# Performance work log

Measured on AMD Instinct MI355X. Metric: run time of the kernel, lower is better.

## Reference

```python
import jax, jax.numpy as jnp
import numpy as np

B, L, D_MODEL, H, HD, FD = 1, 1024, 1024, 16, 64, 64
EPS = 1e-12

def setup_inputs() -> dict:
    key = jax.random.key(0)
    ks = jax.random.split(key, 7)
    s = 1.0 / np.sqrt(D_MODEL)
    return {
        'x': jax.random.normal(ks[0], (B, L, D_MODEL), jnp.float32),
        'Wq': jax.random.normal(ks[1], (D_MODEL, H * HD), jnp.float32) * s,
        'Wk': jax.random.normal(ks[2], (D_MODEL, H * HD), jnp.float32) * s,
        'Wv': jax.random.normal(ks[3], (D_MODEL, H * HD), jnp.float32) * s,
        'Wo': jax.random.normal(ks[4], (H * HD, D_MODEL), jnp.float32) * s,
        'Kq': jax.random.normal(ks[5], (H, HD, FD), jnp.float32) * (1.0 / np.sqrt(HD)),
        'Kk': jax.random.normal(ks[6], (H, HD, FD), jnp.float32) * (1.0 / np.sqrt(HD)),
    }

def _heads(t):
    # (b, l, h*d) -> (b, h, l, d)
    b, l, _ = t.shape
    return t.reshape(b, l, H, HD).transpose(0, 2, 1, 3)

def _feature_map(t, K):
    # UntiedHeadEinsumMLP (no skip) + SoftmaxDim with temp=1.0
    f = jnp.einsum('hdf,bhld->bhlf', K, t)
    feats = jnp.concatenate([jax.nn.softmax(f, axis=-1), jax.nn.softmax(-f, axis=-1)], axis=-1)
    return jnp.maximum(feats, EPS)  # clamp(min=eps)

def reference(x, Wq, Wk, Wv, Wo, Kq, Kk):
    q = _heads(x @ Wq)  # b h l d
    k = _heads(x @ Wk)
    v = _heads(x @ Wv)
    qf = _feature_map(q, Kq)  # b h l 2f
    kf = _feature_map(k, Kk)  # b h l 2f
    # causal linear attention: o_t = phi(q_t) . sum_{s<=t} phi(k_s) v_s^T, normalized
    kv = jnp.cumsum(kf[:, :, :, None, :] * v[..., None], axis=2)  # b h l d 2f
    o = jnp.einsum('bhlf,bhldf->bhld', qf, kv)
    z = jnp.einsum('bhlf,bhlf->bhl', qf, jnp.cumsum(kf, axis=2)) + EPS
    o = o / z[..., None]
    y = o.transpose(0, 2, 1, 3).reshape(x.shape[0], x.shape[1], H * HD)
    return y @ Wo
```

## Files before the change

### kernel.cpp

```cpp
#include <hip/hip_runtime.h>
#include <hip/hip_bf16.h>


#define NH 16
#define NC 16

using short8 = __attribute__((ext_vector_type(8))) short;
using f32x4  = __attribute__((ext_vector_type(4))) float;
typedef const __attribute__((address_space(1))) char* gptr1;
typedef __attribute__((address_space(3))) char* lptr3;

static __device__ __forceinline__ unsigned short bf16bits(float x) {
    __hip_bfloat16 h = __float2bfloat16(x);
    return __builtin_bit_cast(unsigned short, h);
}
static __device__ __forceinline__ float b2f(unsigned short u) {
    return __builtin_bit_cast(float, (unsigned int)u << 16);
}
#define SWZ(row, cb) ((cb) ^ (((row) & 7) << 4))

template<int RS>
static __device__ __forceinline__ short8 ldfrag(const char* buf, int row, int kelem) {
    return *(const short8*)(buf + row * RS + SWZ(row, kelem * 2));
}

__global__ __launch_bounds__(256) void prep(const float* __restrict__ x,
                                            const float* __restrict__ w0,
                                            const float* __restrict__ w1,
                                            const float* __restrict__ w2,
                                            const float* __restrict__ w3,
                                            const float* __restrict__ Kq,
                                            const float* __restrict__ Kk,
                                            __hip_bfloat16* __restrict__ xb,
                                            __hip_bfloat16* __restrict__ d0,
                                            __hip_bfloat16* __restrict__ d1,
                                            __hip_bfloat16* __restrict__ d2,
                                            __hip_bfloat16* __restrict__ d3,
                                            __hip_bfloat16* __restrict__ KqT,
                                            __hip_bfloat16* __restrict__ KkT) {
    const int z = blockIdx.z;
    const int tx = threadIdx.x, ty = threadIdx.y;
    const int tid = ty * 32 + tx;
    if (z < 4) {
        const float* src = (z == 0) ? w0 : (z == 1) ? w1 : (z == 2) ? w2 : w3;
        __hip_bfloat16* dst = (z == 0) ? d0 : (z == 1) ? d1 : (z == 2) ? d2 : d3;
        __shared__ float tile[32][33];
        const int bx = blockIdx.x * 32, by = blockIdx.y * 32;
#pragma unroll
        for (int i = 0; i < 32; i += 8)
            tile[ty + i][tx] = src[(by + ty + i) * 1024 + bx + tx];
        __syncthreads();
#pragma unroll
        for (int i = 0; i < 32; i += 8)
            dst[(size_t)(bx + ty + i) * 1024 + by + tx] = __float2bfloat16(tile[tx][ty + i]);
    } else if (z == 4) {
        const int blk = blockIdx.y * 32 + blockIdx.x;
        const int i = (blk * 256 + tid) * 4;
        float4 v = *(const float4*)(x + i);
        ushort4 o;
        o.x = bf16bits(v.x); o.y = bf16bits(v.y); o.z = bf16bits(v.z); o.w = bf16bits(v.w);
        *(ushort4*)((unsigned short*)xb + i) = o;
    } else {
        if (blockIdx.y != 0 || blockIdx.x >= 32) return;
        const int h = blockIdx.x & 15;
        const float* S = (blockIdx.x >> 4) ? Kk : Kq;
        __hip_bfloat16* D = (blockIdx.x >> 4) ? KkT : KqT;
        __shared__ float t[64][65];
#pragma unroll
        for (int j = 0; j < 16; j++) {
            int e = tid + j * 256, r = e >> 6, c = e & 63;
            t[r][c] = S[h * 4096 + r * 64 + c];
        }
        __syncthreads();
#pragma unroll
        for (int j = 0; j < 16; j++) {
            int e = tid + j * 256, r = e >> 6, c = e & 63;
            D[h * 4096 + r * 64 + c] = __float2bfloat16(t[c][r]);
        }
    }
}

__global__ __launch_bounds__(256) void qkv_feat(const __hip_bfloat16* __restrict__ A,
                                                const __hip_bfloat16* __restrict__ B0,
                                                const __hip_bfloat16* __restrict__ B1,
                                                const __hip_bfloat16* __restrict__ B2,
                                                const __hip_bfloat16* __restrict__ KqT,
                                                const __hip_bfloat16* __restrict__ KkT,
                                                __hip_bfloat16* __restrict__ qf,
                                                __hip_bfloat16* __restrict__ kf,
                                                __hip_bfloat16* __restrict__ kfT,
                                                __hip_bfloat16* __restrict__ VT) {
    __shared__ __align__(16) char smem[49152];
    const int tid = threadIdx.x;
    const int bm = blockIdx.y * 128;
    const int which = blockIdx.x >> 4;
    const int h = blockIdx.x & 15;
    const __hip_bfloat16* B = (which == 0) ? B0 : (which == 1) ? B1 : B2;
    const int bn = h * 64;
    const int wid = tid >> 6, lane = tid & 63;
    const int g = lane >> 4, r16 = lane & 15;
    const char* Ab = (const char*)A;
    const char* Bb = (const char*)B;
    f32x4 acc[2][4] = {};

#define QKV_STAGE(dstA, dstB, kbyte)                                                                   \
    do {                                                                                               \
        _Pragma("unroll") for (int it = 0; it < 4; it++) {                                             \
            const int off = it * 4096 + tid * 16;                                                      \
            const int row = off >> 7, cb = off & 127;                                                  \
            __builtin_amdgcn_global_load_lds((gptr1)(Ab + (size_t)(bm + row) * 2048 + (kbyte) + SWZ(row, cb)), \
                                             (lptr3)((dstA) + it * 4096 + wid * 1024), 16, 0, 0);      \
        }                                                                                              \
        _Pragma("unroll") for (int it = 0; it < 2; it++) {                                             \
            const int off = it * 4096 + tid * 16;                                                      \
            const int row = off >> 7, cb = off & 127;                                                  \
            __builtin_amdgcn_global_load_lds((gptr1)(Bb + (size_t)(bn + row) * 2048 + (kbyte) + SWZ(row, cb)), \
                                             (lptr3)((dstB) + it * 4096 + wid * 1024), 16, 0, 0);      \
        }                                                                                              \
    } while (0)

    QKV_STAGE(smem, smem + 32768, 0);
    for (int kt = 0; kt < 16; kt++) {
        char* Ac = smem + ((kt & 1) ? 16384 : 0);
        char* Bc = smem + 32768 + ((kt & 1) ? 8192 : 0);
        if (kt < 15) {
            char* An = smem + ((kt & 1) ? 0 : 16384);
            char* Bn = smem + 32768 + ((kt & 1) ? 0 : 8192);
            QKV_STAGE(An, Bn, (kt + 1) * 128);
            asm volatile("s_waitcnt vmcnt(6)" ::: "memory");
        } else {
            asm volatile("s_waitcnt vmcnt(0)" ::: "memory");
        }
        __builtin_amdgcn_s_barrier();
#pragma unroll
        for (int ks = 0; ks < 2; ks++) {
            short8 af[2], bfr[4];
#pragma unroll
            for (int m = 0; m < 2; m++)
                af[m] = ldfrag<128>(Ac, wid * 32 + m * 16 + r16, ks * 32 + g * 8);
#pragma unroll
            for (int n = 0; n < 4; n++)
                bfr[n] = ldfrag<128>(Bc, n * 16 + r16, ks * 32 + g * 8);
#pragma unroll
            for (int m = 0; m < 2; m++)
#pragma unroll
                for (int n = 0; n < 4; n++)
                    acc[m][n] = __builtin_amdgcn_mfma_f32_16x16x32_bf16(af[m], bfr[n], acc[m][n], 0, 0, 0);
        }
        asm volatile("s_waitcnt lgkmcnt(0)" ::: "memory");
        __builtin_amdgcn_s_barrier();
    }
#undef QKV_STAGE

    if (which == 2) {
#pragma unroll
        for (int m = 0; m < 2; m++)
#pragma unroll
            for (int n = 0; n < 4; n++) {
                const int col = bn + n * 16 + r16;
                const int row0 = bm + wid * 32 + m * 16 + g * 4;
                ushort4 v;
                v.x = bf16bits(acc[m][n][0]); v.y = bf16bits(acc[m][n][1]);
                v.z = bf16bits(acc[m][n][2]); v.w = bf16bits(acc[m][n][3]);
                *(ushort4*)((unsigned short*)VT + (size_t)col * 1024 + row0) = v;
            }
        return;
    }

    const bool kside = (which == 1);
    char* XS = smem + 32768;
#pragma unroll
    for (int m = 0; m < 2; m++)
#pragma unroll
        for (int n = 0; n < 4; n++)
#pragma unroll
            for (int i = 0; i < 4; i++) {
                const int row = wid * 32 + m * 16 + g * 4 + i;
                *(unsigned short*)(XS + row * 128 + SWZ(row, (n * 16 + r16) * 2)) = bf16bits(acc[m][n][i]);
            }
    {
        const char* KTp = (const char*)(kside ? KkT : KqT);
#pragma unroll
        for (int it = 0; it < 2; it++) {
            const int off = it * 4096 + tid * 16;
            const int row = off >> 7, cb = off & 127;
            __builtin_amdgcn_global_load_lds((gptr1)(KTp + (size_t)(h * 64 + row) * 128 + SWZ(row, cb)),
                                             (lptr3)(smem + it * 4096 + wid * 1024), 16, 0, 0);
        }
    }
    __syncthreads();

    f32x4 fr[2][4] = {};
#pragma unroll
    for (int ks = 0; ks < 2; ks++) {
        short8 af[2], bfr[4];
#pragma unroll
        for (int m = 0; m < 2; m++)
            af[m] = ldfrag<128>(XS, wid * 32 + m * 16 + r16, ks * 32 + g * 8);
#pragma unroll
        for (int n = 0; n < 4; n++)
            bfr[n] = ldfrag<128>(smem, n * 16 + r16, ks * 32 + g * 8);
#pragma unroll
        for (int m = 0; m < 2; m++)
#pragma unroll
            for (int n = 0; n < 4; n++)
                fr[m][n] = __builtin_amdgcn_mfma_f32_16x16x32_bf16(af[m], bfr[n], fr[m][n], 0, 0, 0);
    }
    if (kside) __syncthreads();

    char* ft = smem;
    __hip_bfloat16* feat = kside ? kf : qf;
#pragma unroll
    for (int m = 0; m < 2; m++)
#pragma unroll
        for (int i = 0; i < 4; i++) {
            const int row = wid * 32 + m * 16 + g * 4 + i;
            float m1 = fr[m][0][i], m2 = -fr[m][0][i];
#pragma unroll
            for (int n = 1; n < 4; n++) {
                m1 = fmaxf(m1, fr[m][n][i]);
                m2 = fmaxf(m2, -fr[m][n][i]);
            }
#pragma unroll
            for (int off = 8; off; off >>= 1) {
                m1 = fmaxf(m1, __shfl_xor(m1, off));
                m2 = fmaxf(m2, __shfl_xor(m2, off));
            }
            float e1[4], e2[4], s1 = 0.f, s2 = 0.f;
#pragma unroll
            for (int n = 0; n < 4; n++) {
                e1[n] = __expf(fr[m][n][i] - m1);  s1 += e1[n];
                e2[n] = __expf(-fr[m][n][i] - m2); s2 += e2[n];
            }
#pragma unroll
            for (int off = 8; off; off >>= 1) {
                s1 += __shfl_xor(s1, off);
                s2 += __shfl_xor(s2, off);
            }
            const float i1 = 1.f / s1, i2 = 1.f / s2;
            __hip_bfloat16* fo = feat + ((size_t)(h * 1024 + bm + row)) * 128;
#pragma unroll
            for (int n = 0; n < 4; n++) {
                const int col = n * 16 + r16;
                unsigned short v1 = bf16bits(fmaxf(e1[n] * i1, 1e-12f));
                unsigned short v2 = bf16bits(fmaxf(e2[n] * i2, 1e-12f));
                *(unsigned short*)(fo + col) = v1;
                *(unsigned short*)(fo + col + 64) = v2;
                if (kside) {
                    *(unsigned short*)(ft + col * 256 + SWZ(col, row * 2)) = v1;
                    *(unsigned short*)(ft + (col + 64) * 256 + SWZ(col + 64, row * 2)) = v2;
                }
            }
        }
    if (kside) {
        __syncthreads();
#pragma unroll
        for (int j = 0; j < 8; j++) {
            const int off = (tid + j * 256) * 16;
            const int row = off >> 8, cb = off & 255;
            short8 v = *(const short8*)(ft + row * 256 + SWZ(row, cb));
            *(short8*)((char*)kfT + ((size_t)(h * 128 + row) * 1024 + bm) * 2 + cb) = v;
        }
    }
}

__global__ __launch_bounds__(256) void chunk_sums_mfma(const __hip_bfloat16* __restrict__ kfT,
                                                       const __hip_bfloat16* __restrict__ VT,
                                                       __hip_bfloat16* __restrict__ Scb,
                                                       float* __restrict__ ksum) {
    const int h = blockIdx.y, c = blockIdx.x, l0 = c * 64;
    __shared__ __align__(16) char VTs[64 * 128];
    __shared__ __align__(16) char KTs[128 * 128];
    const int tid = threadIdx.x, lane = tid & 63, wid = tid >> 6;
    const int r16 = lane & 15, g = lane >> 4;
#pragma unroll
    for (int it = 0; it < 2; it++) {
        const int off = it * 4096 + tid * 16;
        const int row = off >> 7, cb = off & 127;
        __builtin_amdgcn_global_load_lds((gptr1)((const char*)VT + ((size_t)(h * 64 + row) * 1024 + l0) * 2 + SWZ(row, cb)),
                                         (lptr3)(VTs + it * 4096 + wid * 1024), 16, 0, 0);
    }
#pragma unroll
    for (int it = 0; it < 4; it++) {
        const int off = it * 4096 + tid * 16;
        const int row = off >> 7, cb = off & 127;
        __builtin_amdgcn_global_load_lds((gptr1)((const char*)kfT + ((size_t)(h * 128 + row) * 1024 + l0) * 2 + SWZ(row, cb)),
                                         (lptr3)(KTs + it * 4096 + wid * 1024), 16, 0, 0);
    }
    __syncthreads();
    f32x4 acc[8] = {};
#pragma unroll
    for (int ks = 0; ks < 2; ks++) {
        short8 a = ldfrag<128>(VTs, wid * 16 + r16, ks * 32 + g * 8);
#pragma unroll
        for (int n = 0; n < 8; n++) {
            short8 b = ldfrag<128>(KTs, n * 16 + r16, ks * 32 + g * 8);
            acc[n] = __builtin_amdgcn_mfma_f32_16x16x32_bf16(a, b, acc[n], 0, 0, 0);
        }
    }
    unsigned short* o = (unsigned short*)Scb + (size_t)(h * NC + c) * 8192;
#pragma unroll
    for (int n = 0; n < 8; n++)
#pragma unroll
        for (int i = 0; i < 4; i++)
            o[(wid * 16 + g * 4 + i) * 128 + n * 16 + r16] = bf16bits(acc[n][i]);
    if (tid < 128) {
        float s = 0.f;
#pragma unroll 8
        for (int t = 0; t < 64; t++)
            s += b2f(*(const unsigned short*)(KTs + tid * 128 + SWZ(tid, t * 2)));
        ksum[(size_t)(h * NC + c) * 128 + tid] = s;
    }
}

__global__ __launch_bounds__(256) void prefix_scan(const __hip_bfloat16* __restrict__ Scb,
                                                   __hip_bfloat16* __restrict__ Sp,
                                                   const float* __restrict__ ksum,
                                                   float* __restrict__ kp) {
    const int h = blockIdx.x, eb = blockIdx.y, tid = threadIdx.x;
#pragma unroll
    for (int j = 0; j < 4; j++) {
        const int e = eb * 1024 + tid + j * 256;
        float v[NC];
#pragma unroll
        for (int c = 0; c < NC; c++)
            v[c] = b2f(((const unsigned short*)Scb)[(size_t)(h * NC + c) * 8192 + e]);
        float run = 0.f;
#pragma unroll
        for (int c = 0; c < NC; c++) {
            Sp[(size_t)(h * NC + c) * 8192 + e] = __float2bfloat16(run);
            run += v[c];
        }
    }
    if (eb == 0 && tid < 128) {
        float run = 0.f;
#pragma unroll
        for (int c = 0; c < NC; c++) {
            const size_t idx = (size_t)(h * NC + c) * 128 + tid;
            kp[idx] = run;
            run += ksum[idx];
        }
    }
}

__global__ __launch_bounds__(256) void chunk_out_mfma(const __hip_bfloat16* __restrict__ qf,
                                                      const __hip_bfloat16* __restrict__ kf,
                                                      const __hip_bfloat16* __restrict__ VT,
                                                      const __hip_bfloat16* __restrict__ Sp,
                                                      const float* __restrict__ kp,
                                                      __hip_bfloat16* __restrict__ Y) {
    const int h = blockIdx.y, c = blockIdx.x, l0 = c * 64;
    __shared__ __align__(16) char QF[64 * 256];
    __shared__ __align__(16) char KF[64 * 256];
    __shared__ __align__(16) char SP[64 * 256];
    __shared__ __align__(16) char VTs[64 * 128];
    __shared__ __align__(16) char AM[64 * 128];
    __shared__ float zi[64];
    __shared__ float invz[64];
    const int tid = threadIdx.x, lane = tid & 63, wid = tid >> 6;
    const int r16 = lane & 15, g = lane >> 4;

#pragma unroll
    for (int it = 0; it < 4; it++) {
        const int off = it * 4096 + wid * 1024 + lane * 16;
        const int row = off >> 8, cb = off & 255;
        const int sw = SWZ(row, cb);
        __builtin_amdgcn_global_load_lds((gptr1)((const char*)qf + ((size_t)(h * 1024 + l0 + row)) * 256 + sw),
                                         (lptr3)(QF + it * 4096 + wid * 1024), 16, 0, 0);
        __builtin_amdgcn_global_load_lds((gptr1)((const char*)kf + ((size_t)(h * 1024 + l0 + row)) * 256 + sw),
                                         (lptr3)(KF + it * 4096 + wid * 1024), 16, 0, 0);
        __builtin_amdgcn_global_load_lds((gptr1)((const char*)Sp + ((size_t)((h * NC + c) * 64 + row)) * 256 + sw),
                                         (lptr3)(SP + it * 4096 + wid * 1024), 16, 0, 0);
    }
#pragma unroll
    for (int it = 0; it < 2; it++) {
        const int off = it * 4096 + wid * 1024 + lane * 16;
        const int row = off >> 7, cb = off & 127;
        __builtin_amdgcn_global_load_lds((gptr1)((const char*)VT + ((size_t)(h * 64 + row) * 1024 + l0) * 2 + SWZ(row, cb)),
                                         (lptr3)(VTs + it * 4096 + wid * 1024), 16, 0, 0);
    }
    __syncthreads();

    f32x4 a4[4] = {};
#pragma unroll
    for (int ks = 0; ks < 4; ks++) {
        short8 a = ldfrag<256>(QF, wid * 16 + r16, ks * 32 + g * 8);
#pragma unroll
        for (int n = 0; n < 4; n++) {
            short8 b = ldfrag<256>(KF, n * 16 + r16, ks * 32 + g * 8);
            a4[n] = __builtin_amdgcn_mfma_f32_16x16x32_bf16(a, b, a4[n], 0, 0, 0);
        }
    }
    const int rowl = wid * 16 + g * 4;
#pragma unroll
    for (int i = 0; i < 4; i++) {
        float r = 0.f;
#pragma unroll
        for (int n = 0; n < 4; n++) {
            const int col = n * 16 + r16;
            float v = (col <= rowl + i) ? a4[n][i] : 0.f;
            a4[n][i] = v;
            r += v;
        }
#pragma unroll
        for (int off = 8; off; off >>= 1) r += __shfl_xor(r, off);
        if (r16 == 0) zi[rowl + i] = r;
#pragma unroll
        for (int n = 0; n < 4; n++)
            *(unsigned short*)(AM + (rowl + i) * 128 + SWZ(rowl + i, (n * 16 + r16) * 2)) = bf16bits(a4[n][i]);
    }
    __syncthreads();

    if (tid < 64) {
        float z = zi[tid] + 1e-12f;
        const float* kpp = kp + (size_t)(h * NC + c) * 128;
#pragma unroll 8
        for (int f = 0; f < 128; f++)
            z += b2f(*(const unsigned short*)(QF + tid * 256 + SWZ(tid, f * 2))) * kpp[f];
        invz[tid] = 1.f / z;
    }

    f32x4 o4[4] = {};
#pragma unroll
    for (int ks = 0; ks < 2; ks++) {
        short8 a = ldfrag<128>(AM, wid * 16 + r16, ks * 32 + g * 8);
#pragma unroll
        for (int n = 0; n < 4; n++) {
            short8 b = ldfrag<128>(VTs, n * 16 + r16, ks * 32 + g * 8);
            o4[n] = __builtin_amdgcn_mfma_f32_16x16x32_bf16(a, b, o4[n], 0, 0, 0);
        }
    }
#pragma unroll
    for (int ks = 0; ks < 4; ks++) {
        short8 a = ldfrag<256>(QF, wid * 16 + r16, ks * 32 + g * 8);
#pragma unroll
        for (int n = 0; n < 4; n++) {
            short8 b = ldfrag<256>(SP, n * 16 + r16, ks * 32 + g * 8);
            o4[n] = __builtin_amdgcn_mfma_f32_16x16x32_bf16(a, b, o4[n], 0, 0, 0);
        }
    }
    __syncthreads();
#pragma unroll
    for (int n = 0; n < 4; n++)
#pragma unroll
        for (int i = 0; i < 4; i++) {
            const int row = rowl + i, col = n * 16 + r16;
            Y[((size_t)(l0 + row)) * 1024 + h * 64 + col] = __float2bfloat16(o4[n][i] * invz[row]);
        }
}

__global__ __launch_bounds__(256) void gemm_final(const __hip_bfloat16* __restrict__ A,
                                                  const __hip_bfloat16* __restrict__ B,
                                                  float* __restrict__ C) {
    __shared__ __align__(16) char smem[32768];
    const int tid = threadIdx.x;
    const int bm = blockIdx.y * 64, bn = blockIdx.x * 64;
    const int wid = tid >> 6, lane = tid & 63;
    const int g = lane >> 4, r16 = lane & 15;
    const int wr = wid >> 1, wc = wid & 1;
    const char* Ab = (const char*)A;
    const char* Bb = (const char*)B;
    f32x4 acc[2][2] = {};

#define FIN_STAGE(dstA, dstB, kbyte)                                                                   \
    do {                                                                                               \
        _Pragma("unroll") for (int it = 0; it < 2; it++) {                                             \
            const int off = it * 4096 + tid * 16;                                                      \
            const int row = off >> 7, cb = off & 127;                                                  \
            __builtin_amdgcn_global_load_lds((gptr1)(Ab + (size_t)(bm + row) * 2048 + (kbyte) + SWZ(row, cb)), \
                                             (lptr3)((dstA) + it * 4096 + wid * 1024), 16, 0, 0);      \
            __builtin_amdgcn_global_load_lds((gptr1)(Bb + (size_t)(bn + row) * 2048 + (kbyte) + SWZ(row, cb)), \
                                             (lptr3)((dstB) + it * 4096 + wid * 1024), 16, 0, 0);      \
        }                                                                                              \
    } while (0)

    FIN_STAGE(smem, smem + 16384, 0);
    for (int kt = 0; kt < 16; kt++) {
        char* Ac = smem + ((kt & 1) ? 8192 : 0);
        char* Bc = smem + 16384 + ((kt & 1) ? 8192 : 0);
        if (kt < 15) {
            char* An = smem + ((kt & 1) ? 0 : 8192);
            char* Bn = smem + 16384 + ((kt & 1) ? 0 : 8192);
            FIN_STAGE(An, Bn, (kt + 1) * 128);
            asm volatile("s_waitcnt vmcnt(4)" ::: "memory");
        } else {
            asm volatile("s_waitcnt vmcnt(0)" ::: "memory");
        }
        __builtin_amdgcn_s_barrier();
#pragma unroll
        for (int ks = 0; ks < 2; ks++) {
            short8 af[2], bfr[2];
#pragma unroll
            for (int m = 0; m < 2; m++)
                af[m] = ldfrag<128>(Ac, wr * 32 + m * 16 + r16, ks * 32 + g * 8);
#pragma unroll
            for (int n = 0; n < 2; n++)
                bfr[n] = ldfrag<128>(Bc, wc * 32 + n * 16 + r16, ks * 32 + g * 8);
#pragma unroll
            for (int m = 0; m < 2; m++)
#pragma unroll
                for (int n = 0; n < 2; n++)
                    acc[m][n] = __builtin_amdgcn_mfma_f32_16x16x32_bf16(af[m], bfr[n], acc[m][n], 0, 0, 0);
        }
        asm volatile("s_waitcnt lgkmcnt(0)" ::: "memory");
        __builtin_amdgcn_s_barrier();
    }
#undef FIN_STAGE
#pragma unroll
    for (int m = 0; m < 2; m++)
#pragma unroll
        for (int n = 0; n < 2; n++)
#pragma unroll
            for (int i = 0; i < 4; i++) {
                const int row = bm + wr * 32 + m * 16 + g * 4 + i;
                const int col = bn + wc * 32 + n * 16 + r16;
                C[(size_t)row * 1024 + col] = acc[m][n][i];
            }
}

extern "C" void kernel_launch(void* const* d_in, const int* in_sizes, int n_in,
                              void* d_out, int out_size, void* d_ws, size_t ws_size,
                              hipStream_t stream) {
    const float* x  = (const float*)d_in[0];
    const float* Wq = (const float*)d_in[1];
    const float* Wk = (const float*)d_in[2];
    const float* Wv = (const float*)d_in[3];
    const float* Wo = (const float*)d_in[4];
    const float* Kq = (const float*)d_in[5];
    const float* Kk = (const float*)d_in[6];
    float* out = (float*)d_out;
    float* ws = (float*)d_ws;

    const size_t M1 = 1024 * 1024;
    if (ws_size < 10 * M1 * sizeof(float)) return;

    __hip_bfloat16* xb  = (__hip_bfloat16*)(ws);
    __hip_bfloat16* Wqt = (__hip_bfloat16*)(ws + M1 / 2);
    __hip_bfloat16* Wkt = (__hip_bfloat16*)(ws + 1 * M1);
    __hip_bfloat16* Wvt = (__hip_bfloat16*)(ws + 3 * M1 / 2);
    __hip_bfloat16* Wot = (__hip_bfloat16*)(ws + 2 * M1);
    __hip_bfloat16* KqT = (__hip_bfloat16*)(ws + 5 * M1 / 2);
    __hip_bfloat16* KkT = (__hip_bfloat16*)(ws + 5 * M1 / 2 + 32768);
    __hip_bfloat16* VT  = (__hip_bfloat16*)(ws + 3 * M1);
    __hip_bfloat16* qfb = (__hip_bfloat16*)(ws + 7 * M1 / 2);
    __hip_bfloat16* kfb = (__hip_bfloat16*)(ws + 9 * M1 / 2);
    __hip_bfloat16* kfT = (__hip_bfloat16*)(ws + 11 * M1 / 2);
    __hip_bfloat16* Scb = (__hip_bfloat16*)(ws + 13 * M1 / 2);
    __hip_bfloat16* Spb = (__hip_bfloat16*)(ws + 15 * M1 / 2);
    __hip_bfloat16* Yb  = (__hip_bfloat16*)(ws + 17 * M1 / 2);
    float* ksum = ws + 9 * M1;
    float* kp   = ws + 9 * M1 + 32768;

    prep<<<dim3(32, 32, 6), dim3(32, 8), 0, stream>>>(x, Wq, Wk, Wv, Wo, Kq, Kk,
                                                      xb, Wqt, Wkt, Wvt, Wot, KqT, KkT);
    qkv_feat<<<dim3(48, 8), 256, 0, stream>>>(xb, Wqt, Wkt, Wvt, KqT, KkT, qfb, kfb, kfT, VT);
    chunk_sums_mfma<<<dim3(NC, NH), 256, 0, stream>>>(kfT, VT, Scb, ksum);
    prefix_scan<<<dim3(NH, 8), 256, 0, stream>>>(Scb, Spb, ksum, kp);
    chunk_out_mfma<<<dim3(NC, NH), 256, 0, stream>>>(qfb, kfb, VT, Spb, kp, Yb);
    gemm_final<<<dim3(16, 16), 256, 0, stream>>>(Yb, Wot, out);
}
```

Measured before the change: 55.26 us.

## Fuse chunk sums, prefix scan and chunk output into one attention kernel

Replaces the three kernels (per-chunk KV sums, cross-chunk prefix scan, chunk output) with one kernel. Each block recomputes the prefix state for its chunk by looping over all earlier chunks, with double-buffered LDS loads and MFMA accumulation. This removes two launches and the global round trips for the per-chunk sums and their prefix, in exchange for redundant work that grows with chunk index (up to 15 chunks for the last blocks), which creates load imbalance.

```diff
diff --git a/kernel.cpp b/kernel.cpp
--- a/kernel.cpp
+++ b/kernel.cpp
@@ -264,15 +264,88 @@
     }
 }
 
-__global__ __launch_bounds__(256) void chunk_sums_mfma(const __hip_bfloat16* __restrict__ kfT,
-                                                       const __hip_bfloat16* __restrict__ VT,
-                                                       __hip_bfloat16* __restrict__ Scb,
-                                                       float* __restrict__ ksum) {
-    const int h = blockIdx.y, c = blockIdx.x, l0 = c * 64;
-    __shared__ __align__(16) char VTs[64 * 128];
-    __shared__ __align__(16) char KTs[128 * 128];
+__global__ __launch_bounds__(256) void chunk_all(const __hip_bfloat16* __restrict__ kfT,
+                                                 const __hip_bfloat16* __restrict__ VT,
+                                                 const __hip_bfloat16* __restrict__ qf,
+                                                 const __hip_bfloat16* __restrict__ kf,
+                                                 __hip_bfloat16* __restrict__ Y) {
+    __shared__ __align__(16) char smem[49152];
+    __shared__ float kpP[2][128];
+    __shared__ float kpL[128];
+    __shared__ float zi[64], invz[64];
+    const int b = blockIdx.x, h = b >> 4, c = b & 15, l0 = c * 64;
     const int tid = threadIdx.x, lane = tid & 63, wid = tid >> 6;
     const int r16 = lane & 15, g = lane >> 4;
+
+    f32x4 accS[8] = {};
+    float kpacc = 0.f;
+    const int fkp = tid & 127, thkp = tid >> 7;
+
+#define CA_STAGE(p, kc)                                                                                 \
+    do {                                                                                                \
+        char* bufp = smem + (p) * 24576;                                                                \
+        _Pragma("unroll") for (int it = 0; it < 2; it++) {                                              \
+            const int off = it * 4096 + tid * 16;                                                       \
+            const int row = off >> 7, cb = off & 127;                                                   \
+            __builtin_amdgcn_global_load_lds((gptr1)((const char*)VT + ((size_t)(h * 64 + row) * 1024 + (kc) * 64) * 2 + SWZ(row, cb)), \
+                                             (lptr3)(bufp + it * 4096 + wid * 1024), 16, 0, 0);         \
+        }                                                                                               \
+        _Pragma("unroll") for (int it = 0; it < 4; it++) {                                              \
+            const int off = it * 4096 + tid * 16;                                                       \
+            const int row = off >> 7, cb = off & 127;                                                   \
+            __builtin_amdgcn_global_load_lds((gptr1)((const char*)kfT + ((size_t)(h * 128 + row) * 1024 + (kc) * 64) * 2 + SWZ(row, cb)), \
+                                             (lptr3)(bufp + 8192 + it * 4096 + wid * 1024), 16, 0, 0);  \
+        }                                                                                               \
+    } while (0)
+
+    if (c > 0) {
+        CA_STAGE(0, 0);
+        for (int kc = 0; kc < c; kc++) {
+            char* VTc = smem + (kc & 1) * 24576;
+            char* KTc = VTc + 8192;
+            if (kc + 1 < c) {
+                CA_STAGE((kc + 1) & 1, kc + 1);
+                asm volatile("s_waitcnt vmcnt(6)" ::: "memory");
+            } else {
+                asm volatile("s_waitcnt vmcnt(0)" ::: "memory");
+            }
+            __builtin_amdgcn_s_barrier();
+#pragma unroll
+            for (int ks = 0; ks < 2; ks++) {
+                short8 a = ldfrag<128>(VTc, wid * 16 + r16, ks * 32 + g * 8);
+#pragma unroll
+                for (int n = 0; n < 8; n++) {
+                    short8 bb = ldfrag<128>(KTc, n * 16 + r16, ks * 32 + g * 8);
+                    accS[n] = __builtin_amdgcn_mfma_f32_16x16x32_bf16(a, bb, accS[n], 0, 0, 0);
+                }
+            }
+#pragma unroll
+            for (int j = 0; j < 4; j++) {
+                short8 v = ldfrag<128>(KTc, fkp, thkp * 32 + j * 8);
+#pragma unroll
+                for (int e = 0; e < 8; e++) kpacc += b2f((unsigned short)v[e]);
+            }
+            asm volatile("s_waitcnt lgkmcnt(0)" ::: "memory");
+            __builtin_amdgcn_s_barrier();
+        }
+    }
+#undef CA_STAGE
+    kpP[thkp][fkp] = kpacc;
+
+    char* QF  = smem;
+    char* KFo = smem + 16384;
+    char* VTs = smem + 32768;
+    char* AM  = smem + 40960;
+#pragma unroll
+    for (int it = 0; it < 4; it++) {
+        const int off = it * 4096 + tid * 16;
+        const int row = off >> 8, cb = off & 255;
+        const int sw = SWZ(row, cb);
+        __builtin_amdgcn_global_load_lds((gptr1)((const char*)qf + ((size_t)(h * 1024 + l0 + row)) * 256 + sw),
+                                         (lptr3)(QF + it * 4096 + wid * 1024), 16, 0, 0);
+        __builtin_amdgcn_global_load_lds((gptr1)((const char*)kf + ((size_t)(h * 1024 + l0 + row)) * 256 + sw),
+                                         (lptr3)(KFo + it * 4096 + wid * 1024), 16, 0, 0);
+    }
 #pragma unroll
     for (int it = 0; it < 2; it++) {
         const int off = it * 4096 + tid * 16;
@@ -280,106 +353,8 @@
         __builtin_amdgcn_global_load_lds((gptr1)((const char*)VT + ((size_t)(h * 64 + row) * 1024 + l0) * 2 + SWZ(row, cb)),
                                          (lptr3)(VTs + it * 4096 + wid * 1024), 16, 0, 0);
     }
-#pragma unroll
-    for (int it = 0; it < 4; it++) {
-        const int off = it * 4096 + tid * 16;
-        const int row = off >> 7, cb = off & 127;
-        __builtin_amdgcn_global_load_lds((gptr1)((const char*)kfT + ((size_t)(h * 128 + row) * 1024 + l0) * 2 + SWZ(row, cb)),
-                                         (lptr3)(KTs + it * 4096 + wid * 1024), 16, 0, 0);
-    }
     __syncthreads();
-    f32x4 acc[8] = {};
-#pragma unroll
-    for (int ks = 0; ks < 2; ks++) {
-        short8 a = ldfrag<128>(VTs, wid * 16 + r16, ks * 32 + g * 8);
-#pragma unroll
-        for (int n = 0; n < 8; n++) {
-            short8 b = ldfrag<128>(KTs, n * 16 + r16, ks * 32 + g * 8);
-            acc[n] = __builtin_amdgcn_mfma_f32_16x16x32_bf16(a, b, acc[n], 0, 0, 0);
-        }
-    }
-    unsigned short* o = (unsigned short*)Scb + (size_t)(h * NC + c) * 8192;
-#pragma unroll
-    for (int n = 0; n < 8; n++)
-#pragma unroll
-        for (int i = 0; i < 4; i++)
-            o[(wid * 16 + g * 4 + i) * 128 + n * 16 + r16] = bf16bits(acc[n][i]);
-    if (tid < 128) {
-        float s = 0.f;
-#pragma unroll 8
-        for (int t = 0; t < 64; t++)
-            s += b2f(*(const unsigned short*)(KTs + tid * 128 + SWZ(tid, t * 2)));
-        ksum[(size_t)(h * NC + c) * 128 + tid] = s;
-    }
-}
-
-__global__ __launch_bounds__(256) void prefix_scan(const __hip_bfloat16* __restrict__ Scb,
-                                                   __hip_bfloat16* __restrict__ Sp,
-                                                   const float* __restrict__ ksum,
-                                                   float* __restrict__ kp) {
-    const int h = blockIdx.x, eb = blockIdx.y, tid = threadIdx.x;
-#pragma unroll
-    for (int j = 0; j < 4; j++) {
-        const int e = eb * 1024 + tid + j * 256;
-        float v[NC];
-#pragma unroll
-        for (int c = 0; c < NC; c++)
-            v[c] = b2f(((const unsigned short*)Scb)[(size_t)(h * NC + c) * 8192 + e]);
-        float run = 0.f;
-#pragma unroll
-        for (int c = 0; c < NC; c++) {
-            Sp[(size_t)(h * NC + c) * 8192 + e] = __float2bfloat16(run);
-            run += v[c];
-        }
-    }
-    if (eb == 0 && tid < 128) {
-        float run = 0.f;
-#pragma unroll
-        for (int c = 0; c < NC; c++) {
-            const size_t idx = (size_t)(h * NC + c) * 128 + tid;
-            kp[idx] = run;
-            run += ksum[idx];
-        }
-    }
-}
-
-__global__ __launch_bounds__(256) void chunk_out_mfma(const __hip_bfloat16* __restrict__ qf,
-                                                      const __hip_bfloat16* __restrict__ kf,
-                                                      const __hip_bfloat16* __restrict__ VT,
-                                                      const __hip_bfloat16* __restrict__ Sp,
-                                                      const float* __restrict__ kp,
-                                                      __hip_bfloat16* __restrict__ Y) {
-    const int h = blockIdx.y, c = blockIdx.x, l0 = c * 64;
-    __shared__ __align__(16) char QF[64 * 256];
-    __shared__ __align__(16) char KF[64 * 256];
-    __shared__ __align__(16) char SP[64 * 256];
-    __shared__ __align__(16) char VTs[64 * 128];
-    __shared__ __align__(16) char AM[64 * 128];
-    __shared__ float zi[64];
-    __shared__ float invz[64];
-    const int tid = threadIdx.x, lane = tid & 63, wid = tid >> 6;
-    const int r16 = lane & 15, g = lane >> 4;
-
-#pragma unroll
-    for (int it = 0; it < 4; it++) {
-        const int off = it * 4096 + wid * 1024 + lane * 16;
-        const int row = off >> 8, cb = off & 255;
-        const int sw = SWZ(row, cb);
-        __builtin_amdgcn_global_load_lds((gptr1)((const char*)qf + ((size_t)(h * 1024 + l0 + row)) * 256 + sw),
-                                         (lptr3)(QF + it * 4096 + wid * 1024), 16, 0, 0);
-        __builtin_amdgcn_global_load_lds((gptr1)((const char*)kf + ((size_t)(h * 1024 + l0 + row)) * 256 + sw),
-                                         (lptr3)(KF + it * 4096 + wid * 1024), 16, 0, 0);
-        __builtin_amdgcn_global_load_lds((gptr1)((const char*)Sp + ((size_t)((h * NC + c) * 64 + row)) * 256 + sw),
-                                         (lptr3)(SP + it * 4096 + wid * 1024), 16, 0, 0);
-    }
-#pragma unroll
-    for (int it = 0; it < 2; it++) {
-        const int off = it * 4096 + wid * 1024 + lane * 16;
-        const int row = off >> 7, cb = off & 127;
-        __builtin_amdgcn_global_load_lds((gptr1)((const char*)VT + ((size_t)(h * 64 + row) * 1024 + l0) * 2 + SWZ(row, cb)),
-                                         (lptr3)(VTs + it * 4096 + wid * 1024), 16, 0, 0);
-    }
-    __syncthreads();
+    if (tid < 128) kpL[tid] = kpP[0][tid] + kpP[1][tid];
 
     f32x4 a4[4] = {};
 #pragma unroll
@@ -387,8 +362,8 @@
         short8 a = ldfrag<256>(QF, wid * 16 + r16, ks * 32 + g * 8);
 #pragma unroll
         for (int n = 0; n < 4; n++) {
-            short8 b = ldfrag<256>(KF, n * 16 + r16, ks * 32 + g * 8);
-            a4[n] = __builtin_amdgcn_mfma_f32_16x16x32_bf16(a, b, a4[n], 0, 0, 0);
+            short8 bb = ldfrag<256>(KFo, n * 16 + r16, ks * 32 + g * 8);
+            a4[n] = __builtin_amdgcn_mfma_f32_16x16x32_bf16(a, bb, a4[n], 0, 0, 0);
         }
     }
     const int rowl = wid * 16 + g * 4;
@@ -411,35 +386,41 @@
     }
     __syncthreads();
 
+    char* SB = KFo;
+#pragma unroll
+    for (int n = 0; n < 8; n++)
+#pragma unroll
+        for (int i = 0; i < 4; i++) {
+            const int d = wid * 16 + g * 4 + i;
+            *(unsigned short*)(SB + d * 256 + SWZ(d, (n * 16 + r16) * 2)) = bf16bits(accS[n][i]);
+        }
     if (tid < 64) {
         float z = zi[tid] + 1e-12f;
-        const float* kpp = kp + (size_t)(h * NC + c) * 128;
 #pragma unroll 8
         for (int f = 0; f < 128; f++)
-            z += b2f(*(const unsigned short*)(QF + tid * 256 + SWZ(tid, f * 2))) * kpp[f];
+            z += b2f(*(const unsigned short*)(QF + tid * 256 + SWZ(tid, f * 2))) * kpL[f];
         invz[tid] = 1.f / z;
     }
-
     f32x4 o4[4] = {};
 #pragma unroll
     for (int ks = 0; ks < 2; ks++) {
         short8 a = ldfrag<128>(AM, wid * 16 + r16, ks * 32 + g * 8);
 #pragma unroll
         for (int n = 0; n < 4; n++) {
-            short8 b = ldfrag<128>(VTs, n * 16 + r16, ks * 32 + g * 8);
-            o4[n] = __builtin_amdgcn_mfma_f32_16x16x32_bf16(a, b, o4[n], 0, 0, 0);
-        }
-    }
+            short8 bb = ldfrag<128>(VTs, n * 16 + r16, ks * 32 + g * 8);
+            o4[n] = __builtin_amdgcn_mfma_f32_16x16x32_bf16(a, bb, o4[n], 0, 0, 0);
+        }
+    }
+    __syncthreads();
 #pragma unroll
     for (int ks = 0; ks < 4; ks++) {
         short8 a = ldfrag<256>(QF, wid * 16 + r16, ks * 32 + g * 8);
 #pragma unroll
         for (int n = 0; n < 4; n++) {
-            short8 b = ldfrag<256>(SP, n * 16 + r16, ks * 32 + g * 8);
-            o4[n] = __builtin_amdgcn_mfma_f32_16x16x32_bf16(a, b, o4[n], 0, 0, 0);
-        }
-    }
-    __syncthreads();
+            short8 bb = ldfrag<256>(SB, n * 16 + r16, ks * 32 + g * 8);
+            o4[n] = __builtin_amdgcn_mfma_f32_16x16x32_bf16(a, bb, o4[n], 0, 0, 0);
+        }
+    }
 #pragma unroll
     for (int n = 0; n < 4; n++)
 #pragma unroll
@@ -532,7 +513,7 @@
     float* ws = (float*)d_ws;
 
     const size_t M1 = 1024 * 1024;
-    if (ws_size < 10 * M1 * sizeof(float)) return;
+    if (ws_size < 8 * M1 * sizeof(float)) return;
 
     __hip_bfloat16* xb  = (__hip_bfloat16*)(ws);
     __hip_bfloat16* Wqt = (__hip_bfloat16*)(ws + M1 / 2);
@@ -545,17 +526,11 @@
     __hip_bfloat16* qfb = (__hip_bfloat16*)(ws + 7 * M1 / 2);
     __hip_bfloat16* kfb = (__hip_bfloat16*)(ws + 9 * M1 / 2);
     __hip_bfloat16* kfT = (__hip_bfloat16*)(ws + 11 * M1 / 2);
-    __hip_bfloat16* Scb = (__hip_bfloat16*)(ws + 13 * M1 / 2);
-    __hip_bfloat16* Spb = (__hip_bfloat16*)(ws + 15 * M1 / 2);
-    __hip_bfloat16* Yb  = (__hip_bfloat16*)(ws + 17 * M1 / 2);
-    float* ksum = ws + 9 * M1;
-    float* kp   = ws + 9 * M1 + 32768;
+    __hip_bfloat16* Yb  = (__hip_bfloat16*)(ws + 13 * M1 / 2);
 
     prep<<<dim3(32, 32, 6), dim3(32, 8), 0, stream>>>(x, Wq, Wk, Wv, Wo, Kq, Kk,
                                                       xb, Wqt, Wkt, Wvt, Wot, KqT, KkT);
     qkv_feat<<<dim3(48, 8), 256, 0, stream>>>(xb, Wqt, Wkt, Wvt, KqT, KkT, qfb, kfb, kfT, VT);
-    chunk_sums_mfma<<<dim3(NC, NH), 256, 0, stream>>>(kfT, VT, Scb, ksum);
-    prefix_scan<<<dim3(NH, 8), 256, 0, stream>>>(Scb, Spb, ksum, kp);
-    chunk_out_mfma<<<dim3(NC, NH), 256, 0, stream>>>(qfb, kfb, VT, Spb, kp, Yb);
+    chunk_all<<<256, 256, 0, stream>>>(kfT, VT, qfb, kfb, Yb);
     gemm_final<<<dim3(16, 16), 256, 0, stream>>>(Yb, Wot, out);
 }
```

Measured after the change: 59.32 us. 7.4% more time.
